# Performance work log

Hardware: AMD Instinct MI355X
Metric: run time of the kernel (lower is better)

Reference implementation:

```python
import jax, jax.numpy as jnp
import numpy as np

N_NODES = 100000
N_EDGES = 3200000
F_IN = 128
NOUT = 32


def _lin(x, W, b):
    return x @ W + b


def _spect_conv(x, src, dst, W, b, n_nodes):
    # edge_attr is all-ones with a single frequency (K=1), so SpectConv reduces to
    # an unweighted scatter-add of linearly transformed source-node features.
    h = x @ W                                   # [N, nout]
    agg = jax.ops.segment_sum(h[src], dst, num_segments=n_nodes)  # [N, nout]
    return agg + b


def setup_inputs() -> dict:
    key = jax.random.key(0)
    ks = jax.random.split(key, 32)
    s = 0.05

    def w(k, shape):
        return jax.random.normal(k, shape, dtype=jnp.float32) * s

    inp = {
        "x": jax.random.normal(ks[0], (N_NODES, F_IN), dtype=jnp.float32),
        "edge_index": jax.random.randint(ks[1], (2, N_EDGES), 0, N_NODES, dtype=jnp.int32),
        # SpectConv weights (single frequency) + biases
        "Wc1": w(ks[2], (F_IN, NOUT)), "bc1": jnp.zeros((NOUT,), jnp.float32),
        "Wc2": w(ks[3], (NOUT, NOUT)), "bc2": jnp.zeros((NOUT,), jnp.float32),
        "Wc3": w(ks[4], (NOUT, NOUT)), "bc3": jnp.zeros((NOUT,), jnp.float32),
        # dense branch weights
        "W11": w(ks[5], (F_IN, NOUT)), "b11": w(ks[6], (NOUT,)),
        "W12": w(ks[7], (F_IN, NOUT)), "b12": w(ks[8], (NOUT,)),
        "W13": w(ks[9], (F_IN, NOUT)), "b13": w(ks[10], (NOUT,)),
        "W21": w(ks[11], (NOUT, NOUT)), "b21": w(ks[12], (NOUT,)),
        "W22": w(ks[13], (NOUT, NOUT)), "b22": w(ks[14], (NOUT,)),
        "W23": w(ks[15], (NOUT, NOUT)), "b23": w(ks[16], (NOUT,)),
        "W31": w(ks[17], (NOUT, NOUT)), "b31": w(ks[18], (NOUT,)),
        "W32": w(ks[19], (NOUT, NOUT)), "b32": w(ks[20], (NOUT,)),
        "W33": w(ks[21], (NOUT, NOUT)), "b33": w(ks[22], (NOUT,)),
        "W2": w(ks[23], (NOUT, 1)), "b2": w(ks[24], (1,)),
    }
    return inp


def reference(x, edge_index,
              Wc1, bc1, Wc2, bc2, Wc3, bc3,
              W11, b11, W12, b12, W13, b13,
              W21, b21, W22, b22, W23, b23,
              W31, b31, W32, b32, W33, b33,
              W2, b2):
    src, dst = edge_index[0], edge_index[1]
    n = x.shape[0]
    relu = jax.nn.relu

    def block(h, Wa, ba, Wc, bc, Wm1, bm1, Wm2, bm2):
        return (relu(_lin(h, Wa, ba))
                + relu(_spect_conv(h, src, dst, Wc, bc, n))
                + relu(_lin(h, Wm1, bm1) * _lin(h, Wm2, bm2)))

    h = block(x, W11, b11, Wc1, bc1, W12, b12, W13, b13)
    h = block(h, W21, b21, Wc2, bc2, W22, b22, W23, b23)
    h = block(h, W31, b31, Wc3, bc3, W32, b32, W33, b33)
    return _lin(h, W2, b2)
```

## Files before the change

kernel.cpp:

```cpp
#include <hip/hip_runtime.h>
#include <hip/hip_bf16.h>
#include <hip/hip_fp8.h>

#define N_FEAT 32
#define CBITS 7
#define CAP   6000
#define TILE  8192

typedef __attribute__((ext_vector_type(8))) short short8;
typedef __attribute__((ext_vector_type(4))) short short4e;
typedef __attribute__((ext_vector_type(4))) float floatx4;

static __device__ __forceinline__ unsigned short f2b(float f) {
    unsigned u = __float_as_uint(f);
    return (unsigned short)((u + 0x7FFFu + ((u >> 16) & 1u)) >> 16);
}
static __device__ __forceinline__ float b2f(unsigned short b) {
    return __uint_as_float(((unsigned)b) << 16);
}
static __device__ __forceinline__ unsigned char f2e(float f) {
    __hip_fp8_e4m3 v(f);
    return (unsigned char)v.__x;
}
static __device__ __forceinline__ float e2f(unsigned char b) {
    __hip_fp8_e4m3 v;
    v.__x = (__hip_fp8_storage_t)b;
    return (float)v;
}

template <int K, bool BF16_IN>
__global__ __launch_bounds__(256)
void transform_mfma_kernel(const void* __restrict__ hin,
                           const float* __restrict__ Wa, const float* __restrict__ ba,
                           const float* __restrict__ Wc,
                           const float* __restrict__ Wm1, const float* __restrict__ bm1,
                           const float* __restrict__ Wm2, const float* __restrict__ bm2,
                           unsigned short* __restrict__ t_pre, unsigned char* __restrict__ t_c,
                           int n_nodes)
{
    constexpr int WPITCH = (K == 32) ? 40 : 136;
    __shared__ unsigned short sW[128][WPITCH];

    const int t = threadIdx.x;
    const int node0 = blockIdx.x * 64;
    const int wave = t >> 6;
    const int lane = t & 63;
    const int m16 = lane & 15;
    const int quad = lane >> 4;

    for (int i = t; i < 128 * K; i += 256) {
        const int c = i & 127, kk = i >> 7;
        const int mat = c >> 5, cl = c & 31;
        const float* W = (mat == 0) ? Wa : (mat == 1) ? Wc : (mat == 2) ? Wm1 : Wm2;
        sW[c][kk] = f2b(W[(size_t)kk * 32 + cl]);
    }
    __syncthreads();

    const int n = node0 + wave * 16 + m16;
    const bool nok = (n < n_nodes);

    floatx4 acc[8];
#pragma unroll
    for (int i = 0; i < 8; ++i) acc[i] = (floatx4){0.f, 0.f, 0.f, 0.f};

#pragma unroll
    for (int k0 = 0; k0 < K; k0 += 32) {
        short8 a;
        if (BF16_IN) {
            const unsigned short* hb = (const unsigned short*)hin;
            a = nok ? *reinterpret_cast<const short8*>(hb + (size_t)n * K + k0 + quad * 8)
                    : (short8){0,0,0,0,0,0,0,0};
        } else {
            const float* hf = (const float*)hin;
            if (nok) {
                const floatx4 v0 = __builtin_nontemporal_load(
                    reinterpret_cast<const floatx4*>(hf + (size_t)n * K + k0 + quad * 8));
                const floatx4 v1 = __builtin_nontemporal_load(
                    reinterpret_cast<const floatx4*>(hf + (size_t)n * K + k0 + quad * 8 + 4));
                union { short8 v; unsigned short u[8]; } pk;
                pk.u[0] = f2b(v0[0]); pk.u[1] = f2b(v0[1]); pk.u[2] = f2b(v0[2]); pk.u[3] = f2b(v0[3]);
                pk.u[4] = f2b(v1[0]); pk.u[5] = f2b(v1[1]); pk.u[6] = f2b(v1[2]); pk.u[7] = f2b(v1[3]);
                a = pk.v;
            } else {
                a = (short8){0,0,0,0,0,0,0,0};
            }
        }
#pragma unroll
        for (int t8 = 0; t8 < 8; ++t8) {
            const short8 b = *reinterpret_cast<const short8*>(&sW[t8 * 16 + m16][k0 + quad * 8]);
            acc[t8] = __builtin_amdgcn_mfma_f32_16x16x32_bf16(a, b, acc[t8], 0, 0, 0);
        }
    }

#pragma unroll
    for (int r = 0; r < 4; ++r) {
        const int node = node0 + wave * 16 + quad * 4 + r;
        if (node < n_nodes) {
#pragma unroll
            for (int half = 0; half < 2; ++half) {
                const int c = m16 + half * 16;
                const float av  = acc[0 + half][r] + ba[c];
                const float wcv = acc[2 + half][r];
                const float m1  = acc[4 + half][r] + bm1[c];
                const float m2  = acc[6 + half][r] + bm2[c];
                t_pre[(size_t)node * N_FEAT + c] = f2b(fmaxf(av, 0.f) + fmaxf(m1 * m2, 0.f));
                t_c[(size_t)node * N_FEAT + c] = f2e(wcv);
            }
        }
    }
}

__global__ __launch_bounds__(1024)
void coarse_bin_kernel(const int* __restrict__ src, const int* __restrict__ dst,
                       unsigned* __restrict__ cnt_g, unsigned* __restrict__ binned,
                       int n_edges, int n_buckets)
{
    __shared__ unsigned sorted[TILE];
    __shared__ unsigned short buck[TILE];
    __shared__ unsigned hist[1024];
    __shared__ unsigned lbase[1024];
    __shared__ unsigned gofs[1024];
    __shared__ unsigned wsum[16], woff[16];

    const int t = threadIdx.x;
    const int wave = t >> 6, lane = t & 63;
    const int e0 = blockIdx.x * TILE;
    const int cnt = min(TILE, n_edges - e0);
    if (cnt <= 0) return;

    hist[t] = 0;
    __syncthreads();

    unsigned dv[TILE / 1024], sv[TILE / 1024];
    int nk = 0;
    for (int i = t; i < cnt; i += 1024, ++nk) {
        dv[nk] = (unsigned)dst[e0 + i];
        sv[nk] = (unsigned)src[e0 + i];
        atomicAdd(&hist[dv[nk] >> CBITS], 1u);
    }
    __syncthreads();

    const unsigned myh = hist[t];
    if (t < n_buckets)
        gofs[t] = myh ? atomicAdd(&cnt_g[t], myh) : 0u;

    unsigned v = myh;
#pragma unroll
    for (int off = 1; off < 64; off <<= 1) {
        const unsigned nv = __shfl_up(v, off);
        if (lane >= off) v += nv;
    }
    if (lane == 63) wsum[wave] = v;
    __syncthreads();
    if (t < 16) {
        unsigned s = wsum[t];
#pragma unroll
        for (int off = 1; off < 16; off <<= 1) {
            const unsigned nv = __shfl_up(s, off, 16);
            if (t >= off) s += nv;
        }
        woff[t] = s - wsum[t];
    }
    hist[t] = 0;
    __syncthreads();
    const unsigned lb_mine = v + woff[wave] - myh;
    lbase[t] = lb_mine;
    __syncthreads();

    for (int k = 0; k < nk; ++k) {
        const unsigned b = dv[k] >> CBITS;
        const unsigned pos = lbase[b] + atomicAdd(&hist[b], 1u);
        sorted[pos] = ((dv[k] & ((1u << CBITS) - 1)) << 17) | sv[k];
        buck[pos] = (unsigned short)b;
    }
    __syncthreads();

    for (int p = t; p < cnt; p += 1024) {
        const unsigned b = buck[p];
        const unsigned gp = gofs[b] + ((unsigned)p - lbase[b]);
        if (gp < CAP) binned[(size_t)b * CAP + gp] = sorted[p];
    }
}

__global__ __launch_bounds__(512)
void fine_sort_kernel(const unsigned* __restrict__ binned,
                      const unsigned* __restrict__ cnt_g,
                      unsigned* __restrict__ total_ctr,
                      int* __restrict__ srcs,
                      unsigned* __restrict__ rowstart, unsigned* __restrict__ rowend,
                      int n_nodes, int n_buckets)
{
    __shared__ int sorted_src[CAP];
    __shared__ unsigned hist[512];
    __shared__ unsigned incl[512];
    __shared__ unsigned ebase[512];
    __shared__ unsigned wsum[8], woff[8];
    __shared__ unsigned ob_s;

    const int t = threadIdx.x;
    const int wave = t >> 6, lane = t & 63;
    const int b = blockIdx.x;
    const unsigned cnt = min(cnt_g[b], (unsigned)CAP);
    const int node0 = b << CBITS;
    const int nodes_here = min(128, n_nodes - node0);
    const unsigned* tile = binned + (size_t)b * CAP;

    if (t == 0) ob_s = atomicAdd(total_ctr, cnt);
    hist[t] = 0;
    __syncthreads();
    const unsigned ob = ob_s;

    for (unsigned i = t; i < cnt; i += 512) {
        const unsigned e = tile[i];
        atomicAdd(&hist[((e >> 17) << 2) | ((e & 0x1FFFFu) >> 15)], 1u);
    }
    __syncthreads();

    const unsigned myh = hist[t];
    unsigned v = myh;
#pragma unroll
    for (int off = 1; off < 64; off <<= 1) {
        const unsigned nv = __shfl_up(v, off);
        if (lane >= off) v += nv;
    }
    if (lane == 63) wsum[wave] = v;
    __syncthreads();
    if (t < 8) {
        unsigned s = wsum[t];
#pragma unroll
        for (int off = 1; off < 8; off <<= 1) {
            const unsigned nv = __shfl_up(s, off, 8);
            if (t >= off) s += nv;
        }
        woff[t] = s - wsum[t];
    }
    hist[t] = 0;
    __syncthreads();
    const unsigned my_incl = v + woff[wave];
    incl[t] = my_incl;
    ebase[t] = my_incl - myh;
    __syncthreads();

    if (t < nodes_here) {
        rowstart[node0 + t] = ob + ebase[t << 2];
        rowend[node0 + t]   = ob + incl[(t << 2) + 3];
    }

    for (unsigned i = t; i < cnt; i += 512) {
        const unsigned e = tile[i];
        const unsigned key = ((e >> 17) << 2) | ((e & 0x1FFFFu) >> 15);
        const unsigned pos = ebase[key] + atomicAdd(&hist[key], 1u);
        sorted_src[pos] = (int)(e & 0x1FFFFu);
    }
    __syncthreads();
    for (unsigned i = t; i < cnt; i += 512)
        srcs[ob + i] = sorted_src[i];
}

static __device__ __forceinline__ void add4e(float* a, unsigned v) {
    a[0] += e2f((unsigned char)(v & 0xffu));
    a[1] += e2f((unsigned char)((v >> 8) & 0xffu));
    a[2] += e2f((unsigned char)((v >> 16) & 0xffu));
    a[3] += e2f((unsigned char)((v >> 24) & 0xffu));
}

__global__ __launch_bounds__(512)
void gather_transform_kernel(const unsigned char* __restrict__ t_c_in,
                             const unsigned short* __restrict__ t_pre_in,
                             const unsigned* __restrict__ rowstart,
                             const unsigned* __restrict__ rowend,
                             const int* __restrict__ srcs,
                             const float* __restrict__ bc,
                             const float* __restrict__ Wa, const float* __restrict__ ba,
                             const float* __restrict__ Wc,
                             const float* __restrict__ Wm1, const float* __restrict__ bm1,
                             const float* __restrict__ Wm2, const float* __restrict__ bm2,
                             unsigned short* __restrict__ t_pre_out,
                             unsigned char* __restrict__ t_c_out,
                             int n_nodes)
{
    __shared__ unsigned short sW[128][40];
    __shared__ unsigned short sH[64][40];

    const int t = threadIdx.x;
    const int node0 = blockIdx.x * 64;

    for (int i = t; i < 128 * 32; i += 512) {
        const int c = i & 127, kk = i >> 7;
        const int mat = c >> 5, cl = c & 31;
        const float* W = (mat == 0) ? Wa : (mat == 1) ? Wc : (mat == 2) ? Wm1 : Wm2;
        sW[c][kk] = f2b(W[(size_t)kk * 32 + cl]);
    }

    const int nl = t >> 3;
    const int node = node0 + nl;
    const int l8 = t & 7;
    const int f0 = l8 * 4;
    const bool nvalid = (node < n_nodes);

    if (nvalid) {
        const unsigned lo = rowstart[node], hi = rowend[node];
        float acc[4] = {0.f, 0.f, 0.f, 0.f};
        unsigned i = lo;

        if (i + 8 <= hi) {
            int sp[8];
#pragma unroll
            for (int j = 0; j < 8; ++j) sp[j] = srcs[i + j];
            for (;;) {
                unsigned v[8];
#pragma unroll
                for (int j = 0; j < 8; ++j)
                    v[j] = *reinterpret_cast<const unsigned*>(t_c_in + (size_t)sp[j] * N_FEAT + f0);
                i += 8;
                const bool more = (i + 8 <= hi);
                int sn[8];
#pragma unroll
                for (int j = 0; j < 8; ++j) {
                    const unsigned idx = more ? (i + j) : (hi - 1);
                    sn[j] = srcs[idx];
                }
#pragma unroll
                for (int j = 0; j < 8; ++j) add4e(acc, v[j]);
#pragma unroll
                for (int j = 0; j < 8; ++j) sp[j] = sn[j];
                if (!more) break;
            }
        }
        for (; i + 4 <= hi; i += 4) {
            unsigned v[4];
#pragma unroll
            for (int j = 0; j < 4; ++j)
                v[j] = *reinterpret_cast<const unsigned*>(
                    t_c_in + (size_t)srcs[i + j] * N_FEAT + f0);
#pragma unroll
            for (int j = 0; j < 4; ++j) add4e(acc, v[j]);
        }
        for (; i < hi; ++i)
            add4e(acc, *reinterpret_cast<const unsigned*>(
                t_c_in + (size_t)srcs[i] * N_FEAT + f0));

        const short4e p = *reinterpret_cast<const short4e*>(t_pre_in + (size_t)node * N_FEAT + f0);
        union { short4e v; unsigned short u[4]; } r;
#pragma unroll
        for (int j = 0; j < 4; ++j)
            r.u[j] = f2b(b2f((unsigned short)p[j]) + fmaxf(acc[j] + bc[f0 + j], 0.f));
        *reinterpret_cast<short4e*>(&sH[nl][f0]) = r.v;
    } else {
        *reinterpret_cast<short4e*>(&sH[nl][f0]) = (short4e){0, 0, 0, 0};
    }
    __syncthreads();

    const int wave = t >> 6;
    if (wave < 4) {
        const int lane = t & 63;
        const int m16 = lane & 15;
        const int quad = lane >> 4;

        floatx4 acc2[8];
#pragma unroll
        for (int i = 0; i < 8; ++i) acc2[i] = (floatx4){0.f, 0.f, 0.f, 0.f};

        const short8 a = *reinterpret_cast<const short8*>(&sH[wave * 16 + m16][quad * 8]);
#pragma unroll
        for (int t8 = 0; t8 < 8; ++t8) {
            const short8 b = *reinterpret_cast<const short8*>(&sW[t8 * 16 + m16][quad * 8]);
            acc2[t8] = __builtin_amdgcn_mfma_f32_16x16x32_bf16(a, b, acc2[t8], 0, 0, 0);
        }

#pragma unroll
        for (int r = 0; r < 4; ++r) {
            const int onode = node0 + wave * 16 + quad * 4 + r;
            if (onode < n_nodes) {
#pragma unroll
                for (int half = 0; half < 2; ++half) {
                    const int c = m16 + half * 16;
                    const float av  = acc2[0 + half][r] + ba[c];
                    const float wcv = acc2[2 + half][r];
                    const float m1  = acc2[4 + half][r] + bm1[c];
                    const float m2  = acc2[6 + half][r] + bm2[c];
                    t_pre_out[(size_t)onode * N_FEAT + c] = f2b(fmaxf(av, 0.f) + fmaxf(m1 * m2, 0.f));
                    t_c_out[(size_t)onode * N_FEAT + c] = f2e(wcv);
                }
            }
        }
    }
}

__global__ __launch_bounds__(256)
void gather_final_kernel(const unsigned char* __restrict__ t_c,
                         const unsigned short* __restrict__ t_pre,
                         const unsigned* __restrict__ rowstart,
                         const unsigned* __restrict__ rowend,
                         const int* __restrict__ srcs,
                         const float* __restrict__ bc, const float* __restrict__ W2,
                         const float* __restrict__ b2, float* __restrict__ out,
                         int n_nodes)
{
    const int node = blockIdx.x * 32 + (threadIdx.x >> 3);
    const int l8 = threadIdx.x & 7;
    const int f0 = l8 * 4;
    if (node >= n_nodes) return;
    const unsigned lo = rowstart[node], hi = rowend[node];
    float acc[4] = {0.f, 0.f, 0.f, 0.f};
    unsigned i = lo;

    if (i + 8 <= hi) {
        int sp[8];
#pragma unroll
        for (int j = 0; j < 8; ++j) sp[j] = srcs[i + j];
        for (;;) {
            unsigned v[8];
#pragma unroll
            for (int j = 0; j < 8; ++j)
                v[j] = *reinterpret_cast<const unsigned*>(t_c + (size_t)sp[j] * N_FEAT + f0);
            i += 8;
            const bool more = (i + 8 <= hi);
            int sn[8];
#pragma unroll
            for (int j = 0; j < 8; ++j) {
                const unsigned idx = more ? (i + j) : (hi - 1);
                sn[j] = srcs[idx];
            }
#pragma unroll
            for (int j = 0; j < 8; ++j) add4e(acc, v[j]);
#pragma unroll
            for (int j = 0; j < 8; ++j) sp[j] = sn[j];
            if (!more) break;
        }
    }
    for (; i + 4 <= hi; i += 4) {
        unsigned v[4];
#pragma unroll
        for (int j = 0; j < 4; ++j)
            v[j] = *reinterpret_cast<const unsigned*>(
                t_c + (size_t)srcs[i + j] * N_FEAT + f0);
#pragma unroll
        for (int j = 0; j < 4; ++j) add4e(acc, v[j]);
    }
    for (; i < hi; ++i)
        add4e(acc, *reinterpret_cast<const unsigned*>(
            t_c + (size_t)srcs[i] * N_FEAT + f0));

    const short4e p = *reinterpret_cast<const short4e*>(t_pre + (size_t)node * N_FEAT + f0);
    float r = 0.f;
#pragma unroll
    for (int j = 0; j < 4; ++j)
        r += (b2f((unsigned short)p[j]) + fmaxf(acc[j] + bc[f0 + j], 0.f)) * W2[f0 + j];
    r += __shfl_down(r, 4, 8);
    r += __shfl_down(r, 2, 8);
    r += __shfl_down(r, 1, 8);
    if (l8 == 0) out[node] = r + b2[0];
}

extern "C" void kernel_launch(void* const* d_in, const int* in_sizes, int n_in,
                              void* d_out, int out_size, void* d_ws, size_t ws_size,
                              hipStream_t stream)
{
    const float* x   = (const float*)d_in[0];
    const int*   ei  = (const int*)d_in[1];
    const float* Wc1 = (const float*)d_in[2];  const float* bc1 = (const float*)d_in[3];
    const float* Wc2 = (const float*)d_in[4];  const float* bc2 = (const float*)d_in[5];
    const float* Wc3 = (const float*)d_in[6];  const float* bc3 = (const float*)d_in[7];
    const float* W11 = (const float*)d_in[8];  const float* b11 = (const float*)d_in[9];
    const float* W12 = (const float*)d_in[10]; const float* b12 = (const float*)d_in[11];
    const float* W13 = (const float*)d_in[12]; const float* b13 = (const float*)d_in[13];
    const float* W21 = (const float*)d_in[14]; const float* b21 = (const float*)d_in[15];
    const float* W22 = (const float*)d_in[16]; const float* b22 = (const float*)d_in[17];
    const float* W23 = (const float*)d_in[18]; const float* b23 = (const float*)d_in[19];
    const float* W31 = (const float*)d_in[20]; const float* b31 = (const float*)d_in[21];
    const float* W32 = (const float*)d_in[22]; const float* b32 = (const float*)d_in[23];
    const float* W33 = (const float*)d_in[24]; const float* b33 = (const float*)d_in[25];
    const float* W2  = (const float*)d_in[26]; const float* b2  = (const float*)d_in[27];

    const int n_nodes = in_sizes[0] / 128;
    const int n_edges = in_sizes[1] / 2;
    const int* src = ei;
    const int* dst = ei + n_edges;
    const int n_buckets = (n_nodes + (1 << CBITS) - 1) >> CBITS;

    const size_t feat_elems = (size_t)n_nodes * N_FEAT;

    unsigned short* tpreA    = (unsigned short*)d_ws;
    unsigned short* tpreB    = tpreA + feat_elems;
    unsigned char*  tcA      = (unsigned char*)(tpreB + feat_elems);
    unsigned char*  tcB      = tcA + feat_elems;
    int*            srcs     = (int*)(tcB + feat_elems);
    unsigned*       rowstart = (unsigned*)(srcs + n_edges);
    unsigned*       rowend   = rowstart + n_nodes;
    unsigned*       cnt_g    = rowend + n_nodes;
    unsigned*       binned   = cnt_g + (n_buckets + 1);

    const int tf_grid = (n_nodes + 63) / 64;
    const int gt_grid = (n_nodes + 63) / 64;
    const int gf_grid = (n_nodes + 31) / 32;
    const int cb_grid = (n_edges + TILE - 1) / TILE;

    hipMemsetAsync(cnt_g, 0, ((size_t)n_buckets + 1) * sizeof(unsigned), stream);
    coarse_bin_kernel<<<cb_grid, 1024, 0, stream>>>(src, dst, cnt_g, binned, n_edges, n_buckets);
    fine_sort_kernel<<<n_buckets, 512, 0, stream>>>(
        binned, cnt_g, cnt_g + n_buckets, srcs, rowstart, rowend, n_nodes, n_buckets);

    transform_mfma_kernel<128, false><<<tf_grid, 256, 0, stream>>>(
        x, W11, b11, Wc1, W12, b12, W13, b13, tpreA, tcA, n_nodes);

    gather_transform_kernel<<<gt_grid, 512, 0, stream>>>(
        tcA, tpreA, rowstart, rowend, srcs, bc1,
        W21, b21, Wc2, W22, b22, W23, b23, tpreB, tcB, n_nodes);

    gather_transform_kernel<<<gt_grid, 512, 0, stream>>>(
        tcB, tpreB, rowstart, rowend, srcs, bc2,
        W31, b31, Wc3, W32, b32, W33, b33, tpreA, tcA, n_nodes);

    gather_final_kernel<<<gf_grid, 256, 0, stream>>>(
        tcA, tpreA, rowstart, rowend, srcs, bc3, W2, b2, (float*)d_out, n_nodes);
}
```

Measured before the change: 298.4 us.

## Fuse all stages into a cooperative persistent megakernel with grid syncs

```diff
diff --git a/kernel.cpp b/kernel.cpp
--- a/kernel.cpp
+++ b/kernel.cpp
@@ -1,15 +1,20 @@
 #include <hip/hip_runtime.h>
 #include <hip/hip_bf16.h>
 #include <hip/hip_fp8.h>
+#include <hip/hip_cooperative_groups.h>
+
+namespace cg = cooperative_groups;
 
 #define N_FEAT 32
 #define CBITS 7
 #define CAP   6000
 #define TILE  8192
+#define NT    1024
 
 typedef __attribute__((ext_vector_type(8))) short short8;
 typedef __attribute__((ext_vector_type(4))) short short4e;
 typedef __attribute__((ext_vector_type(4))) float floatx4;
+typedef __attribute__((ext_vector_type(2))) float floatx2;
 
 static __device__ __forceinline__ unsigned short f2b(float f) {
     unsigned u = __float_as_uint(f);
@@ -27,32 +32,191 @@
     v.__x = (__hip_fp8_storage_t)b;
     return (float)v;
 }
-
-template <int K, bool BF16_IN>
-__global__ __launch_bounds__(256)
-void transform_mfma_kernel(const void* __restrict__ hin,
-                           const float* __restrict__ Wa, const float* __restrict__ ba,
-                           const float* __restrict__ Wc,
-                           const float* __restrict__ Wm1, const float* __restrict__ bm1,
-                           const float* __restrict__ Wm2, const float* __restrict__ bm2,
-                           unsigned short* __restrict__ t_pre, unsigned char* __restrict__ t_c,
-                           int n_nodes)
-{
-    constexpr int WPITCH = (K == 32) ? 40 : 136;
-    __shared__ unsigned short sW[128][WPITCH];
-
+static __device__ __forceinline__ void add4e(float* a, unsigned v) {
+#if defined(__has_builtin) && __has_builtin(__builtin_amdgcn_cvt_pk_f32_fp8)
+    const floatx2 lo = __builtin_amdgcn_cvt_pk_f32_fp8((int)v, false);
+    const floatx2 hi = __builtin_amdgcn_cvt_pk_f32_fp8((int)v, true);
+    a[0] += lo[0]; a[1] += lo[1]; a[2] += hi[0]; a[3] += hi[1];
+#else
+    a[0] += e2f((unsigned char)(v & 0xffu));
+    a[1] += e2f((unsigned char)((v >> 8) & 0xffu));
+    a[2] += e2f((unsigned char)((v >> 16) & 0xffu));
+    a[3] += e2f((unsigned char)((v >> 24) & 0xffu));
+#endif
+}
+
+union SmemU {
+    struct {
+        unsigned sorted[TILE];
+        unsigned short buck[TILE];
+        unsigned hist[1024];
+        unsigned lbase[1024];
+        unsigned gofs[1024];
+        unsigned wsum[16], woff[16];
+    } cb;
+    struct {
+        int sorted_src[CAP];
+        unsigned hist[512], incl[512], ebase[512];
+        unsigned wsum[8], woff[8];
+        unsigned ob;
+    } fs;
+    struct { unsigned short sW[128][136]; } t1;
+    struct { unsigned short sW[128][40]; unsigned short sH[128][40]; } gt;
+};
+
+
+static __device__ void cb_body(SmemU* s, int tile, const int* __restrict__ src,
+                               const int* __restrict__ dst, unsigned* cnt_g,
+                               unsigned* binned, int n_edges, int n_buckets)
+{
+    auto& c = s->cb;
     const int t = threadIdx.x;
-    const int node0 = blockIdx.x * 64;
-    const int wave = t >> 6;
-    const int lane = t & 63;
-    const int m16 = lane & 15;
-    const int quad = lane >> 4;
-
-    for (int i = t; i < 128 * K; i += 256) {
+    const int wave = t >> 6, lane = t & 63;
+    const int e0 = tile * TILE;
+    const int cnt = min(TILE, n_edges - e0);
+    if (cnt <= 0) return;
+
+    c.hist[t] = 0;
+    __syncthreads();
+
+    unsigned dv[TILE / NT], sv[TILE / NT];
+    int nk = 0;
+    for (int i = t; i < cnt; i += NT, ++nk) {
+        dv[nk] = (unsigned)dst[e0 + i];
+        sv[nk] = (unsigned)src[e0 + i];
+        atomicAdd(&c.hist[dv[nk] >> CBITS], 1u);
+    }
+    __syncthreads();
+
+    const unsigned myh = c.hist[t];
+    if (t < n_buckets)
+        c.gofs[t] = myh ? atomicAdd(&cnt_g[t], myh) : 0u;
+
+    unsigned v = myh;
+#pragma unroll
+    for (int off = 1; off < 64; off <<= 1) {
+        const unsigned nv = __shfl_up(v, off);
+        if (lane >= off) v += nv;
+    }
+    if (lane == 63) c.wsum[wave] = v;
+    __syncthreads();
+    if (t < 16) {
+        unsigned ss = c.wsum[t];
+#pragma unroll
+        for (int off = 1; off < 16; off <<= 1) {
+            const unsigned nv = __shfl_up(ss, off, 16);
+            if (t >= off) ss += nv;
+        }
+        c.woff[t] = ss - c.wsum[t];
+    }
+    c.hist[t] = 0;
+    __syncthreads();
+    c.lbase[t] = v + c.woff[wave] - myh;
+    __syncthreads();
+
+    for (int k = 0; k < nk; ++k) {
+        const unsigned b = dv[k] >> CBITS;
+        const unsigned pos = c.lbase[b] + atomicAdd(&c.hist[b], 1u);
+        c.sorted[pos] = ((dv[k] & ((1u << CBITS) - 1)) << 17) | sv[k];
+        c.buck[pos] = (unsigned short)b;
+    }
+    __syncthreads();
+
+    for (int p = t; p < cnt; p += NT) {
+        const unsigned b = c.buck[p];
+        const unsigned gp = c.gofs[b] + ((unsigned)p - c.lbase[b]);
+        if (gp < CAP) binned[(size_t)b * CAP + gp] = c.sorted[p];
+    }
+}
+
+static __device__ void fine_body(SmemU* s, int b, const unsigned* __restrict__ binned,
+                                 const unsigned* __restrict__ cnt_g, unsigned* total_ctr,
+                                 int* srcs, unsigned* rowstart, unsigned* rowend,
+                                 int n_nodes)
+{
+    auto& f = s->fs;
+    const int t = threadIdx.x;
+    const int wave = t >> 6, lane = t & 63;
+    const unsigned cnt = min(cnt_g[b], (unsigned)CAP);
+    const int node0 = b << CBITS;
+    const int nodes_here = min(128, n_nodes - node0);
+    const unsigned* tile = binned + (size_t)b * CAP;
+
+    if (t == 0) f.ob = atomicAdd(total_ctr, cnt);
+    if (t < 512) f.hist[t] = 0;
+    __syncthreads();
+    const unsigned ob = f.ob;
+
+    for (unsigned i = t; i < cnt; i += NT) {
+        const unsigned e = tile[i];
+        atomicAdd(&f.hist[((e >> 17) << 2) | ((e & 0x1FFFFu) >> 15)], 1u);
+    }
+    __syncthreads();
+
+    unsigned myh = 0, v = 0;
+    if (t < 512) {
+        myh = f.hist[t];
+        v = myh;
+#pragma unroll
+        for (int off = 1; off < 64; off <<= 1) {
+            const unsigned nv = __shfl_up(v, off);
+            if (lane >= off) v += nv;
+        }
+        if (lane == 63) f.wsum[wave] = v;
+    }
+    __syncthreads();
+    if (t < 8) {
+        unsigned ss = f.wsum[t];
+#pragma unroll
+        for (int off = 1; off < 8; off <<= 1) {
+            const unsigned nv = __shfl_up(ss, off, 8);
+            if (t >= off) ss += nv;
+        }
+        f.woff[t] = ss - f.wsum[t];
+    }
+    if (t < 512) f.hist[t] = 0;
+    __syncthreads();
+    if (t < 512) {
+        const unsigned mi = v + f.woff[wave];
+        f.incl[t] = mi;
+        f.ebase[t] = mi - myh;
+    }
+    __syncthreads();
+
+    if (t < nodes_here) {
+        rowstart[node0 + t] = ob + f.ebase[t << 2];
+        rowend[node0 + t]   = ob + f.incl[(t << 2) + 3];
+    }
+
+    for (unsigned i = t; i < cnt; i += NT) {
+        const unsigned e = tile[i];
+        const unsigned key = ((e >> 17) << 2) | ((e & 0x1FFFFu) >> 15);
+        const unsigned pos = f.ebase[key] + atomicAdd(&f.hist[key], 1u);
+        f.sorted_src[pos] = (int)(e & 0x1FFFFu);
+    }
+    __syncthreads();
+    for (unsigned i = t; i < cnt; i += NT)
+        srcs[ob + i] = f.sorted_src[i];
+}
+
+static __device__ void t1_body(SmemU* s, int unit, const float* __restrict__ x,
+                               const float* __restrict__ Wa, const float* __restrict__ ba,
+                               const float* __restrict__ Wc,
+                               const float* __restrict__ Wm1, const float* __restrict__ bm1,
+                               const float* __restrict__ Wm2, const float* __restrict__ bm2,
+                               unsigned short* t_pre, unsigned char* t_c, int n_nodes)
+{
+    auto& w = s->t1;
+    const int t = threadIdx.x;
+    const int node0 = unit * 256;
+    const int wave = t >> 6, lane = t & 63;
+    const int m16 = lane & 15, quad = lane >> 4;
+
+    for (int i = t; i < 128 * 128; i += NT) {
         const int c = i & 127, kk = i >> 7;
         const int mat = c >> 5, cl = c & 31;
         const float* W = (mat == 0) ? Wa : (mat == 1) ? Wc : (mat == 2) ? Wm1 : Wm2;
-        sW[c][kk] = f2b(W[(size_t)kk * 32 + cl]);
+        w.sW[c][kk] = f2b(W[(size_t)kk * 32 + cl]);
     }
     __syncthreads();
 
@@ -64,30 +228,21 @@
     for (int i = 0; i < 8; ++i) acc[i] = (floatx4){0.f, 0.f, 0.f, 0.f};
 
 #pragma unroll
-    for (int k0 = 0; k0 < K; k0 += 32) {
+    for (int k0 = 0; k0 < 128; k0 += 32) {
         short8 a;
-        if (BF16_IN) {
-            const unsigned short* hb = (const unsigned short*)hin;
-            a = nok ? *reinterpret_cast<const short8*>(hb + (size_t)n * K + k0 + quad * 8)
-                    : (short8){0,0,0,0,0,0,0,0};
+        if (nok) {
+            const float4 v0 = *reinterpret_cast<const float4*>(x + (size_t)n * 128 + k0 + quad * 8);
+            const float4 v1 = *reinterpret_cast<const float4*>(x + (size_t)n * 128 + k0 + quad * 8 + 4);
+            union { short8 v; unsigned short u[8]; } pk;
+            pk.u[0] = f2b(v0.x); pk.u[1] = f2b(v0.y); pk.u[2] = f2b(v0.z); pk.u[3] = f2b(v0.w);
+            pk.u[4] = f2b(v1.x); pk.u[5] = f2b(v1.y); pk.u[6] = f2b(v1.z); pk.u[7] = f2b(v1.w);
+            a = pk.v;
         } else {
-            const float* hf = (const float*)hin;
-            if (nok) {
-                const floatx4 v0 = __builtin_nontemporal_load(
-                    reinterpret_cast<const floatx4*>(hf + (size_t)n * K + k0 + quad * 8));
-                const floatx4 v1 = __builtin_nontemporal_load(
-                    reinterpret_cast<const floatx4*>(hf + (size_t)n * K + k0 + quad * 8 + 4));
-                union { short8 v; unsigned short u[8]; } pk;
-                pk.u[0] = f2b(v0[0]); pk.u[1] = f2b(v0[1]); pk.u[2] = f2b(v0[2]); pk.u[3] = f2b(v0[3]);
-                pk.u[4] = f2b(v1[0]); pk.u[5] = f2b(v1[1]); pk.u[6] = f2b(v1[2]); pk.u[7] = f2b(v1[3]);
-                a = pk.v;
-            } else {
-                a = (short8){0,0,0,0,0,0,0,0};
-            }
+            a = (short8){0,0,0,0,0,0,0,0};
         }
 #pragma unroll
         for (int t8 = 0; t8 < 8; ++t8) {
-            const short8 b = *reinterpret_cast<const short8*>(&sW[t8 * 16 + m16][k0 + quad * 8]);
+            const short8 b = *reinterpret_cast<const short8*>(&w.sW[t8 * 16 + m16][k0 + quad * 8]);
             acc[t8] = __builtin_amdgcn_mfma_f32_16x16x32_bf16(a, b, acc[t8], 0, 0, 0);
         }
     }
@@ -110,195 +265,39 @@
     }
 }
 
-__global__ __launch_bounds__(1024)
-void coarse_bin_kernel(const int* __restrict__ src, const int* __restrict__ dst,
-                       unsigned* __restrict__ cnt_g, unsigned* __restrict__ binned,
-                       int n_edges, int n_buckets)
-{
-    __shared__ unsigned sorted[TILE];
-    __shared__ unsigned short buck[TILE];
-    __shared__ unsigned hist[1024];
-    __shared__ unsigned lbase[1024];
-    __shared__ unsigned gofs[1024];
-    __shared__ unsigned wsum[16], woff[16];
-
+static __device__ void gstage_weights(SmemU* s, const float* Wa, const float* Wc,
+                                      const float* Wm1, const float* Wm2)
+{
     const int t = threadIdx.x;
-    const int wave = t >> 6, lane = t & 63;
-    const int e0 = blockIdx.x * TILE;
-    const int cnt = min(TILE, n_edges - e0);
-    if (cnt <= 0) return;
-
-    hist[t] = 0;
-    __syncthreads();
-
-    unsigned dv[TILE / 1024], sv[TILE / 1024];
-    int nk = 0;
-    for (int i = t; i < cnt; i += 1024, ++nk) {
-        dv[nk] = (unsigned)dst[e0 + i];
-        sv[nk] = (unsigned)src[e0 + i];
-        atomicAdd(&hist[dv[nk] >> CBITS], 1u);
-    }
-    __syncthreads();
-
-    const unsigned myh = hist[t];
-    if (t < n_buckets)
-        gofs[t] = myh ? atomicAdd(&cnt_g[t], myh) : 0u;
-
-    unsigned v = myh;
-#pragma unroll
-    for (int off = 1; off < 64; off <<= 1) {
-        const unsigned nv = __shfl_up(v, off);
-        if (lane >= off) v += nv;
-    }
-    if (lane == 63) wsum[wave] = v;
-    __syncthreads();
-    if (t < 16) {
-        unsigned s = wsum[t];
-#pragma unroll
-        for (int off = 1; off < 16; off <<= 1) {
-            const unsigned nv = __shfl_up(s, off, 16);
-            if (t >= off) s += nv;
-        }
-        woff[t] = s - wsum[t];
-    }
-    hist[t] = 0;
-    __syncthreads();
-    const unsigned lb_mine = v + woff[wave] - myh;
-    lbase[t] = lb_mine;
-    __syncthreads();
-
-    for (int k = 0; k < nk; ++k) {
-        const unsigned b = dv[k] >> CBITS;
-        const unsigned pos = lbase[b] + atomicAdd(&hist[b], 1u);
-        sorted[pos] = ((dv[k] & ((1u << CBITS) - 1)) << 17) | sv[k];
-        buck[pos] = (unsigned short)b;
-    }
-    __syncthreads();
-
-    for (int p = t; p < cnt; p += 1024) {
-        const unsigned b = buck[p];
-        const unsigned gp = gofs[b] + ((unsigned)p - lbase[b]);
-        if (gp < CAP) binned[(size_t)b * CAP + gp] = sorted[p];
-    }
-}
-
-__global__ __launch_bounds__(512)
-void fine_sort_kernel(const unsigned* __restrict__ binned,
-                      const unsigned* __restrict__ cnt_g,
-                      unsigned* __restrict__ total_ctr,
-                      int* __restrict__ srcs,
-                      unsigned* __restrict__ rowstart, unsigned* __restrict__ rowend,
-                      int n_nodes, int n_buckets)
-{
-    __shared__ int sorted_src[CAP];
-    __shared__ unsigned hist[512];
-    __shared__ unsigned incl[512];
-    __shared__ unsigned ebase[512];
-    __shared__ unsigned wsum[8], woff[8];
-    __shared__ unsigned ob_s;
-
-    const int t = threadIdx.x;
-    const int wave = t >> 6, lane = t & 63;
-    const int b = blockIdx.x;
-    const unsigned cnt = min(cnt_g[b], (unsigned)CAP);
-    const int node0 = b << CBITS;
-    const int nodes_here = min(128, n_nodes - node0);
-    const unsigned* tile = binned + (size_t)b * CAP;
-
-    if (t == 0) ob_s = atomicAdd(total_ctr, cnt);
-    hist[t] = 0;
-    __syncthreads();
-    const unsigned ob = ob_s;
-
-    for (unsigned i = t; i < cnt; i += 512) {
-        const unsigned e = tile[i];
-        atomicAdd(&hist[((e >> 17) << 2) | ((e & 0x1FFFFu) >> 15)], 1u);
-    }
-    __syncthreads();
-
-    const unsigned myh = hist[t];
-    unsigned v = myh;
-#pragma unroll
-    for (int off = 1; off < 64; off <<= 1) {
-        const unsigned nv = __shfl_up(v, off);
-        if (lane >= off) v += nv;
-    }
-    if (lane == 63) wsum[wave] = v;
-    __syncthreads();
-    if (t < 8) {
-        unsigned s = wsum[t];
-#pragma unroll
-        for (int off = 1; off < 8; off <<= 1) {
-            const unsigned nv = __shfl_up(s, off, 8);
-            if (t >= off) s += nv;
-        }
-        woff[t] = s - wsum[t];
-    }
-    hist[t] = 0;
-    __syncthreads();
-    const unsigned my_incl = v + woff[wave];
-    incl[t] = my_incl;
-    ebase[t] = my_incl - myh;
-    __syncthreads();
-
-    if (t < nodes_here) {
-        rowstart[node0 + t] = ob + ebase[t << 2];
-        rowend[node0 + t]   = ob + incl[(t << 2) + 3];
-    }
-
-    for (unsigned i = t; i < cnt; i += 512) {
-        const unsigned e = tile[i];
-        const unsigned key = ((e >> 17) << 2) | ((e & 0x1FFFFu) >> 15);
-        const unsigned pos = ebase[key] + atomicAdd(&hist[key], 1u);
-        sorted_src[pos] = (int)(e & 0x1FFFFu);
-    }
-    __syncthreads();
-    for (unsigned i = t; i < cnt; i += 512)
-        srcs[ob + i] = sorted_src[i];
-}
-
-static __device__ __forceinline__ void add4e(float* a, unsigned v) {
-    a[0] += e2f((unsigned char)(v & 0xffu));
-    a[1] += e2f((unsigned char)((v >> 8) & 0xffu));
-    a[2] += e2f((unsigned char)((v >> 16) & 0xffu));
-    a[3] += e2f((unsigned char)((v >> 24) & 0xffu));
-}
-
-__global__ __launch_bounds__(512)
-void gather_transform_kernel(const unsigned char* __restrict__ t_c_in,
-                             const unsigned short* __restrict__ t_pre_in,
-                             const unsigned* __restrict__ rowstart,
-                             const unsigned* __restrict__ rowend,
-                             const int* __restrict__ srcs,
-                             const float* __restrict__ bc,
-                             const float* __restrict__ Wa, const float* __restrict__ ba,
-                             const float* __restrict__ Wc,
-                             const float* __restrict__ Wm1, const float* __restrict__ bm1,
-                             const float* __restrict__ Wm2, const float* __restrict__ bm2,
-                             unsigned short* __restrict__ t_pre_out,
-                             unsigned char* __restrict__ t_c_out,
-                             int n_nodes)
-{
-    __shared__ unsigned short sW[128][40];
-    __shared__ unsigned short sH[64][40];
-
-    const int t = threadIdx.x;
-    const int node0 = blockIdx.x * 64;
-
-    for (int i = t; i < 128 * 32; i += 512) {
+    for (int i = t; i < 128 * 32; i += NT) {
         const int c = i & 127, kk = i >> 7;
         const int mat = c >> 5, cl = c & 31;
         const float* W = (mat == 0) ? Wa : (mat == 1) ? Wc : (mat == 2) ? Wm1 : Wm2;
-        sW[c][kk] = f2b(W[(size_t)kk * 32 + cl]);
-    }
-
+        s->gt.sW[c][kk] = f2b(W[(size_t)kk * 32 + cl]);
+    }
+}
+
+static __device__ void gather_unit(SmemU* s, int unit,
+                                   const unsigned char* __restrict__ t_c_in,
+                                   const unsigned short* __restrict__ t_pre_in,
+                                   const unsigned* __restrict__ rowstart,
+                                   const unsigned* __restrict__ rowend,
+                                   const int* __restrict__ srcs,
+                                   const float* __restrict__ bc,
+                                   const float* __restrict__ ba,
+                                   const float* __restrict__ bm1,
+                                   const float* __restrict__ bm2,
+                                   unsigned short* t_pre_out, unsigned char* t_c_out,
+                                   int n_nodes)
+{
+    auto& g = s->gt;
+    const int t = threadIdx.x;
+    const int node0 = unit * 128;
     const int nl = t >> 3;
     const int node = node0 + nl;
-    const int l8 = t & 7;
-    const int f0 = l8 * 4;
-    const bool nvalid = (node < n_nodes);
-
-    if (nvalid) {
+    const int l8 = t & 7, f0 = l8 * 4;
+
+    if (node < n_nodes) {
         const unsigned lo = rowstart[node], hi = rowend[node];
         float acc[4] = {0.f, 0.f, 0.f, 0.f};
         unsigned i = lo;
@@ -331,40 +330,37 @@
             unsigned v[4];
 #pragma unroll
             for (int j = 0; j < 4; ++j)
-                v[j] = *reinterpret_cast<const unsigned*>(
-                    t_c_in + (size_t)srcs[i + j] * N_FEAT + f0);
+                v[j] = *reinterpret_cast<const unsigned*>(t_c_in + (size_t)srcs[i + j] * N_FEAT + f0);
 #pragma unroll
             for (int j = 0; j < 4; ++j) add4e(acc, v[j]);
         }
         for (; i < hi; ++i)
-            add4e(acc, *reinterpret_cast<const unsigned*>(
-                t_c_in + (size_t)srcs[i] * N_FEAT + f0));
+            add4e(acc, *reinterpret_cast<const unsigned*>(t_c_in + (size_t)srcs[i] * N_FEAT + f0));
 
         const short4e p = *reinterpret_cast<const short4e*>(t_pre_in + (size_t)node * N_FEAT + f0);
         union { short4e v; unsigned short u[4]; } r;
 #pragma unroll
         for (int j = 0; j < 4; ++j)
             r.u[j] = f2b(b2f((unsigned short)p[j]) + fmaxf(acc[j] + bc[f0 + j], 0.f));
-        *reinterpret_cast<short4e*>(&sH[nl][f0]) = r.v;
+        *reinterpret_cast<short4e*>(&g.sH[nl][f0]) = r.v;
     } else {
-        *reinterpret_cast<short4e*>(&sH[nl][f0]) = (short4e){0, 0, 0, 0};
+        *reinterpret_cast<short4e*>(&g.sH[nl][f0]) = (short4e){0, 0, 0, 0};
     }
     __syncthreads();
 
     const int wave = t >> 6;
-    if (wave < 4) {
+    if (wave < 8) {
         const int lane = t & 63;
-        const int m16 = lane & 15;
-        const int quad = lane >> 4;
+        const int m16 = lane & 15, quad = lane >> 4;
 
         floatx4 acc2[8];
 #pragma unroll
         for (int i = 0; i < 8; ++i) acc2[i] = (floatx4){0.f, 0.f, 0.f, 0.f};
 
-        const short8 a = *reinterpret_cast<const short8*>(&sH[wave * 16 + m16][quad * 8]);
+        const short8 a = *reinterpret_cast<const short8*>(&g.sH[wave * 16 + m16][quad * 8]);
 #pragma unroll
         for (int t8 = 0; t8 < 8; ++t8) {
-            const short8 b = *reinterpret_cast<const short8*>(&sW[t8 * 16 + m16][quad * 8]);
+            const short8 b = *reinterpret_cast<const short8*>(&g.sW[t8 * 16 + m16][quad * 8]);
             acc2[t8] = __builtin_amdgcn_mfma_f32_16x16x32_bf16(a, b, acc2[t8], 0, 0, 0);
         }
 
@@ -385,21 +381,20 @@
             }
         }
     }
-}
-
-__global__ __launch_bounds__(256)
-void gather_final_kernel(const unsigned char* __restrict__ t_c,
-                         const unsigned short* __restrict__ t_pre,
-                         const unsigned* __restrict__ rowstart,
-                         const unsigned* __restrict__ rowend,
-                         const int* __restrict__ srcs,
-                         const float* __restrict__ bc, const float* __restrict__ W2,
-                         const float* __restrict__ b2, float* __restrict__ out,
-                         int n_nodes)
-{
-    const int node = blockIdx.x * 32 + (threadIdx.x >> 3);
-    const int l8 = threadIdx.x & 7;
-    const int f0 = l8 * 4;
+    __syncthreads();
+}
+
+static __device__ void gf_body(int unit, const unsigned char* __restrict__ t_c,
+                               const unsigned short* __restrict__ t_pre,
+                               const unsigned* __restrict__ rowstart,
+                               const unsigned* __restrict__ rowend,
+                               const int* __restrict__ srcs,
+                               const float* __restrict__ bc, const float* __restrict__ W2,
+                               const float* __restrict__ b2, float* out, int n_nodes)
+{
+    const int t = threadIdx.x;
+    const int node = unit * 128 + (t >> 3);
+    const int l8 = t & 7, f0 = l8 * 4;
     if (node >= n_nodes) return;
     const unsigned lo = rowstart[node], hi = rowend[node];
     float acc[4] = {0.f, 0.f, 0.f, 0.f};
@@ -433,14 +428,12 @@
         unsigned v[4];
 #pragma unroll
         for (int j = 0; j < 4; ++j)
-            v[j] = *reinterpret_cast<const unsigned*>(
-                t_c + (size_t)srcs[i + j] * N_FEAT + f0);
+            v[j] = *reinterpret_cast<const unsigned*>(t_c + (size_t)srcs[i + j] * N_FEAT + f0);
 #pragma unroll
         for (int j = 0; j < 4; ++j) add4e(acc, v[j]);
     }
     for (; i < hi; ++i)
-        add4e(acc, *reinterpret_cast<const unsigned*>(
-            t_c + (size_t)srcs[i] * N_FEAT + f0));
+        add4e(acc, *reinterpret_cast<const unsigned*>(t_c + (size_t)srcs[i] * N_FEAT + f0));
 
     const short4e p = *reinterpret_cast<const short4e*>(t_pre + (size_t)node * N_FEAT + f0);
     float r = 0.f;
@@ -451,6 +444,118 @@
     r += __shfl_down(r, 2, 8);
     r += __shfl_down(r, 1, 8);
     if (l8 == 0) out[node] = r + b2[0];
+}
+
+
+struct MegaArgs {
+    const float* x; const int* src; const int* dst;
+    const float *bc1, *bc2, *bc3;
+    const float *W11, *b11, *Wc1, *W12, *b12, *W13, *b13;
+    const float *W21, *b21, *Wc2, *W22, *b22, *W23, *b23;
+    const float *W31, *b31, *Wc3, *W32, *b32, *W33, *b33;
+    const float *W2, *b2;
+    unsigned short *tpreA, *tpreB;
+    unsigned char *tcA, *tcB;
+    int* srcs; unsigned *rowstart, *rowend, *cnt_g, *binned;
+    float* out;
+    int n_nodes, n_edges, n_buckets;
+};
+
+__global__ __launch_bounds__(NT, 8)
+void mega_kernel(MegaArgs a)
+{
+    __shared__ SmemU smem;
+    cg::grid_group grid = cg::this_grid();
+    const int bid = blockIdx.x, nb = gridDim.x;
+    const int t = threadIdx.x;
+
+    for (int i = bid * NT + t; i < a.n_buckets + 1; i += nb * NT) a.cnt_g[i] = 0;
+    grid.sync();
+
+    const int ntiles = (a.n_edges + TILE - 1) / TILE;
+    for (int u = bid; u < ntiles; u += nb) {
+        __syncthreads();
+        cb_body(&smem, u, a.src, a.dst, a.cnt_g, a.binned, a.n_edges, a.n_buckets);
+    }
+    grid.sync();
+
+    const int t1u = (a.n_nodes + 255) / 256;
+    for (int u = bid; u < a.n_buckets + t1u; u += nb) {
+        __syncthreads();
+        if (u < a.n_buckets)
+            fine_body(&smem, u, a.binned, a.cnt_g, a.cnt_g + a.n_buckets,
+                      a.srcs, a.rowstart, a.rowend, a.n_nodes);
+        else
+            t1_body(&smem, u - a.n_buckets, a.x, a.W11, a.b11, a.Wc1,
+                    a.W12, a.b12, a.W13, a.b13, a.tpreA, a.tcA, a.n_nodes);
+    }
+    grid.sync();
+
+    const int gu = (a.n_nodes + 127) / 128;
+
+    __syncthreads();
+    gstage_weights(&smem, a.W21, a.Wc2, a.W22, a.W23);
+    for (int u = bid; u < gu; u += nb)
+        gather_unit(&smem, u, a.tcA, a.tpreA, a.rowstart, a.rowend, a.srcs, a.bc1,
+                    a.b21, a.b22, a.b23, a.tpreB, a.tcB, a.n_nodes);
+    grid.sync();
+
+    __syncthreads();
+    gstage_weights(&smem, a.W31, a.Wc3, a.W32, a.W33);
+    for (int u = bid; u < gu; u += nb)
+        gather_unit(&smem, u, a.tcB, a.tpreB, a.rowstart, a.rowend, a.srcs, a.bc2,
+                    a.b31, a.b32, a.b33, a.tpreA, a.tcA, a.n_nodes);
+    grid.sync();
+
+    for (int u = bid; u < gu; u += nb)
+        gf_body(u, a.tcA, a.tpreA, a.rowstart, a.rowend, a.srcs,
+                a.bc3, a.W2, a.b2, a.out, a.n_nodes);
+}
+
+
+__global__ __launch_bounds__(NT, 8)
+void cb_kernel(const int* src, const int* dst, unsigned* cnt_g, unsigned* binned,
+               int n_edges, int n_buckets)
+{
+    __shared__ SmemU smem;
+    cb_body(&smem, blockIdx.x, src, dst, cnt_g, binned, n_edges, n_buckets);
+}
+
+__global__ __launch_bounds__(NT, 8)
+void fine_t1_kernel(const unsigned* binned, const unsigned* cnt_g, unsigned* total_ctr,
+                    int* srcs, unsigned* rowstart, unsigned* rowend,
+                    int n_nodes, int n_buckets,
+                    const float* x, const float* Wa, const float* ba, const float* Wc,
+                    const float* Wm1, const float* bm1, const float* Wm2, const float* bm2,
+                    unsigned short* t_pre, unsigned char* t_c)
+{
+    __shared__ SmemU smem;
+    const int u = blockIdx.x;
+    if (u < n_buckets)
+        fine_body(&smem, u, binned, cnt_g, total_ctr, srcs, rowstart, rowend, n_nodes);
+    else
+        t1_body(&smem, u - n_buckets, x, Wa, ba, Wc, Wm1, bm1, Wm2, bm2, t_pre, t_c, n_nodes);
+}
+
+__global__ __launch_bounds__(NT, 8)
+void gt_kernel(const unsigned char* t_c_in, const unsigned short* t_pre_in,
+               const unsigned* rowstart, const unsigned* rowend, const int* srcs,
+               const float* bc, const float* Wa, const float* ba, const float* Wc,
+               const float* Wm1, const float* bm1, const float* Wm2, const float* bm2,
+               unsigned short* t_pre_out, unsigned char* t_c_out, int n_nodes)
+{
+    __shared__ SmemU smem;
+    gstage_weights(&smem, Wa, Wc, Wm1, Wm2);
+    gather_unit(&smem, blockIdx.x, t_c_in, t_pre_in, rowstart, rowend, srcs, bc,
+                ba, bm1, bm2, t_pre_out, t_c_out, n_nodes);
+}
+
+__global__ __launch_bounds__(NT, 8)
+void gf_kernel(const unsigned char* t_c, const unsigned short* t_pre,
+               const unsigned* rowstart, const unsigned* rowend, const int* srcs,
+               const float* bc, const float* W2, const float* b2, float* out, int n_nodes)
+{
+    gf_body(blockIdx.x, t_c, t_pre, rowstart, rowend, srcs, bc, W2, b2, out, n_nodes);
 }
 
 extern "C" void kernel_launch(void* const* d_in, const int* in_sizes, int n_in,
@@ -491,27 +596,45 @@
     unsigned*       cnt_g    = rowend + n_nodes;
     unsigned*       binned   = cnt_g + (n_buckets + 1);
 
-    const int tf_grid = (n_nodes + 63) / 64;
-    const int gt_grid = (n_nodes + 63) / 64;
-    const int gf_grid = (n_nodes + 31) / 32;
-    const int cb_grid = (n_edges + TILE - 1) / TILE;
+    MegaArgs a;
+    a.x = x; a.src = src; a.dst = dst;
+    a.bc1 = bc1; a.bc2 = bc2; a.bc3 = bc3;
+    a.W11 = W11; a.b11 = b11; a.Wc1 = Wc1; a.W12 = W12; a.b12 = b12; a.W13 = W13; a.b13 = b13;
+    a.W21 = W21; a.b21 = b21; a.Wc2 = Wc2; a.W22 = W22; a.b22 = b22; a.W23 = W23; a.b23 = b23;
+    a.W31 = W31; a.b31 = b31; a.Wc3 = Wc3; a.W32 = W32; a.b32 = b32; a.W33 = W33; a.b33 = b33;
+    a.W2 = W2; a.b2 = b2;
+    a.tpreA = tpreA; a.tpreB = tpreB; a.tcA = tcA; a.tcB = tcB;
+    a.srcs = srcs; a.rowstart = rowstart; a.rowend = rowend; a.cnt_g = cnt_g; a.binned = binned;
+    a.out = (float*)d_out;
+    a.n_nodes = n_nodes; a.n_edges = n_edges; a.n_buckets = n_buckets;
+
+    const int ntiles  = (n_edges + TILE - 1) / TILE;
+    const int t1u     = (n_nodes + 255) / 256;
+    const int gu      = (n_nodes + 127) / 128;
+
+    int occ = 0;
+    hipError_t oe = hipOccupancyMaxActiveBlocksPerMultiprocessor(&occ, mega_kernel, NT, 0);
+    if (oe == hipSuccess && occ >= 1) {
+        int nblocks = occ * 256;
+        int maxwork = n_buckets + t1u;
+        if (gu > maxwork) maxwork = gu;
+        if (ntiles > maxwork) maxwork = ntiles;
+        if (nblocks > maxwork) nblocks = maxwork;
+        void* params[] = { (void*)&a };
+        hipError_t le = hipLaunchCooperativeKernel((const void*)mega_kernel,
+                                                   dim3(nblocks), dim3(NT), params, 0, stream);
+        if (le == hipSuccess) return;
+    }
 
     hipMemsetAsync(cnt_g, 0, ((size_t)n_buckets + 1) * sizeof(unsigned), stream);
-    coarse_bin_kernel<<<cb_grid, 1024, 0, stream>>>(src, dst, cnt_g, binned, n_edges, n_buckets);
-    fine_sort_kernel<<<n_buckets, 512, 0, stream>>>(
-        binned, cnt_g, cnt_g + n_buckets, srcs, rowstart, rowend, n_nodes, n_buckets);
-
-    transform_mfma_kernel<128, false><<<tf_grid, 256, 0, stream>>>(
-        x, W11, b11, Wc1, W12, b12, W13, b13, tpreA, tcA, n_nodes);
-
-    gather_transform_kernel<<<gt_grid, 512, 0, stream>>>(
-        tcA, tpreA, rowstart, rowend, srcs, bc1,
-        W21, b21, Wc2, W22, b22, W23, b23, tpreB, tcB, n_nodes);
-
-    gather_transform_kernel<<<gt_grid, 512, 0, stream>>>(
-        tcB, tpreB, rowstart, rowend, srcs, bc2,
-        W31, b31, Wc3, W32, b32, W33, b33, tpreA, tcA, n_nodes);
-
-    gather_final_kernel<<<gf_grid, 256, 0, stream>>>(
-        tcA, tpreA, rowstart, rowend, srcs, bc3, W2, b2, (float*)d_out, n_nodes);
-}
+    cb_kernel<<<ntiles, NT, 0, stream>>>(src, dst, cnt_g, binned, n_edges, n_buckets);
+    fine_t1_kernel<<<n_buckets + t1u, NT, 0, stream>>>(
+        binned, cnt_g, cnt_g + n_buckets, srcs, rowstart, rowend, n_nodes, n_buckets,
+        x, W11, b11, Wc1, W12, b12, W13, b13, tpreA, tcA);
+    gt_kernel<<<gu, NT, 0, stream>>>(tcA, tpreA, rowstart, rowend, srcs, bc1,
+                                     W21, b21, Wc2, W22, b22, W23, b23, tpreB, tcB, n_nodes);
+    gt_kernel<<<gu, NT, 0, stream>>>(tcB, tpreB, rowstart, rowend, srcs, bc2,
+                                     W31, b31, Wc3, W32, b32, W33, b33, tpreA, tcA, n_nodes);
+    gf_kernel<<<gu, NT, 0, stream>>>(tcA, tpreA, rowstart, rowend, srcs, bc3,
+                                     W2, b2, (float*)d_out, n_nodes);
+}
```

Measured after the change: 548.9 us. 84.0% more time.
